# Optimization experiments

Hardware: AMD Instinct MI355X
Metric: run time of the kernel (lower is better)

Reference implementation:

```python
import jax, jax.numpy as jnp
import numpy as np


def setup_inputs() -> dict:
    key = jax.random.key(0)
    k1, k2, k3, k4, k5 = jax.random.split(key, 5)
    N, M, K = 200000, 50, 4
    T = 1000.0
    ti = jnp.sort(jax.random.uniform(k1, (N,), dtype=jnp.float32) * T)
    mi = jax.random.randint(k2, (N,), 0, M, dtype=jnp.int64)
    mu_at_events = jax.random.uniform(k3, (N,), dtype=jnp.float32) * 0.5 + 0.05
    alpha = jax.random.uniform(k4, (K, M, M), dtype=jnp.float32) * 0.1
    gamma = jax.random.uniform(k5, (K,), dtype=jnp.float32) * 2.0 + 0.5
    return {"ti": ti, "mi": mi, "mu_at_events": mu_at_events, "alpha": alpha, "gamma": gamma}


def _hawkes_logsum(ti, mi, mu_at_events, alpha, gamma):
    # ti: [N] sorted event times; mi: [N] event types in [0, M)
    # alpha: [K, M, M]; gamma: [K]; mu_at_events: [N]
    N = ti.shape[0]
    M = alpha.shape[1]
    # inter-event gaps; dt[0] = 0 so the first event has zero excitation state
    dt = jnp.concatenate([jnp.zeros((1,), ti.dtype), ti[1:] - ti[:-1]])  # [N]
    a = jnp.exp(-gamma[None, :] * dt[:, None])  # [N, K] decay factors
    # one-hot of the PREVIOUS event's type (row 0 is all-zero, matching e_mi)
    prev_onehot = jnp.zeros((N, M), ti.dtype).at[jnp.arange(1, N), mi[:-1]].set(1.0)
    b = a[:, None, :] * prev_onehot[:, :, None]  # [N, M, K]

    # linear recurrence S_i = a_i * S_{i-1} + b_i via associative scan
    # combine((a1,b1),(a2,b2)) = (a1*a2, a2*b1 + b2)
    def combine(x, y):
        a1, b1 = x
        a2, b2 = y
        return (a1 * a2, a2[:, None, :] * b1 + b2)

    _, S = jax.lax.associative_scan(combine, (a, b))  # S: [N, M, K]
    # S[i, m, k] = sum_{j < i, m_j = m} exp(-gamma_k (t_i - t_j))
    alpha_at = alpha[:, mi, :]  # [K, N, M] rows of alpha for each event's type
    lam = mu_at_events + jnp.einsum('knm,nmk,k->n', alpha_at, S, gamma)  # [N]
    return jnp.sum(jnp.log(lam))


def reference(ti, mi, mu_at_events, alpha, gamma):
    return _hawkes_logsum(ti, mi, mu_at_events, alpha, gamma)
```

## Files before the change

### kernel.cpp

```cpp
#include <hip/hip_runtime.h>

#define CHUNK 256
#define MM 50
#define KK 4
#define STATE 200
#define ASTRIDE 51
#define SUP 32
#define NSMAX 26
#define GMAX 1024

__device__ int   g_ticket;
__device__ float g_chunkB[GMAX * STATE];
__device__ float g_superB[64 * STATE];

__device__ __forceinline__ unsigned short f2bf(float x) {
  unsigned u = __float_as_uint(x);
  u += 0x7fffu + ((u >> 16) & 1u);
  return (unsigned short)(u >> 16);
}
__device__ __forceinline__ float bflo(unsigned u) { return __uint_as_float(u << 16); }
__device__ __forceinline__ float bfhi(unsigned u) { return __uint_as_float(u & 0xffff0000u); }

__device__ __forceinline__ void st_agent(float* p, float v) {
  __hip_atomic_store(p, v, __ATOMIC_RELAXED, __HIP_MEMORY_SCOPE_AGENT);
}
__device__ __forceinline__ float ld_agent(const float* p) {
  return __hip_atomic_load(p, __ATOMIC_RELAXED, __HIP_MEMORY_SCOPE_AGENT);
}

__global__ __launch_bounds__(512) void hawkes_df(
    const float* __restrict__ ti, const int* __restrict__ mi,
    const float* __restrict__ mu, const float* __restrict__ alpha,
    const float* __restrict__ gamma, float* __restrict__ out,
    int N, int G, int NB) {
  int tid = threadIdx.x;
  __shared__ int vid_s;
  __shared__ unsigned P0[MM * ASTRIDE];
  __shared__ unsigned P1[MM * ASTRIDE];
  __shared__ __align__(16) float4 Fj[512];
  __shared__ int   cj[512];
  __shared__ __align__(16) float Q[16][STATE];
  __shared__ float SB1[STATE];
  __shared__ float SB2[STATE];
  __shared__ float teL[SUP];
  __shared__ float tlast[NSMAX];
  __shared__ float red8[8];

  if (tid == 0) vid_s = atomicAdd(&g_ticket, 1);

  int b = blockIdx.x;
  int c0 = 2 * b;
  int lQ = c0 * CHUNK;
  int sup = b >> 4;
  int g0c = sup * SUP;
  int nloc = c0 - g0c;
  int ch = tid >> 8;

  float gk0 = gamma[0], gk1 = gamma[1], gk2 = gamma[2], gk3 = gamma[3];

  for (int i = tid; i < 16 * STATE; i += 512) ((float*)Q)[i] = 0.f;
  if (tid < SUP) {
    int c = g0c + tid;
    if (c < G) teL[tid] = ti[min(N, (c + 1) * CHUNK) - 1];
  } else if (tid >= 64 && tid < 64 + NSMAX) {
    int s = tid - 64;
    if (s < sup) tlast[s] = ti[min(N, (s + 1) * SUP * CHUNK) - 1];
  }
  if (b == 0 && tid == 0) st_agent(out, 0.f);

  float tref0 = ti[(b == 0) ? 0 : (lQ - 1)];
  float tref_ch = ch ? ti[min(N - 1, lQ + CHUNK - 1)] : tref0;
  int n = lQ + tid;
  bool has_n = (n < N);
  float ti_n = has_n ? ti[n] : 0.f;
  int   mi_n = has_n ? mi[n] : 0;
  float mu_n = has_n ? mu[n] : 0.f;
  int j = lQ - 1 + tid;
  float ti_j = __shfl_up(ti_n, 1, 64);
  int   mi_j = __shfl_up(mi_n, 1, 64);
  if ((tid & 63) == 0 && j >= 0) { ti_j = ti[j]; mi_j = mi[j]; }
  bool valid = (j >= 0) && has_n;
  int myc = valid ? mi_j : 0;
  float4 F = make_float4(0.f, 0.f, 0.f, 0.f);
  if (valid) {
    float tj = ti_j - tref_ch;
    F = make_float4(__expf(gk0 * tj), __expf(gk1 * tj),
                    __expf(gk2 * tj), __expf(gk3 * tj));
  }
  cj[tid] = myc;
  Fj[tid] = F;
  __syncthreads();

  if (valid) {
    float* q = &Q[tid >> 5][myc * KK];
    atomicAdd(q + 0, F.x); atomicAdd(q + 1, F.y);
    atomicAdd(q + 2, F.z); atomicAdd(q + 3, F.w);
  }
  #pragma unroll
  for (int u = 0; u < 5; ++u) {
    int idx = tid + 512 * u;
    if (idx < MM * MM) {
      int c = idx / MM, cp = idx - c * MM;
      float a0 = gk0 * alpha[idx];
      float a1 = gk1 * alpha[2500 + idx];
      float a2 = gk2 * alpha[5000 + idx];
      float a3 = gk3 * alpha[7500 + idx];
      P0[c * ASTRIDE + cp] = (unsigned)f2bf(a0) | ((unsigned)f2bf(a1) << 16);
      P1[c * ASTRIDE + cp] = (unsigned)f2bf(a2) | ((unsigned)f2bf(a3) << 16);
    }
  }
  __syncthreads();

  float epoch_s = ((vid_s / NB) & 1) ? -1.f : 1.f;
  float gkc = (tid & 2) ? ((tid & 1) ? gk3 : gk2) : ((tid & 1) ? gk1 : gk0);
  float totA = 0.f, totB = 0.f, dA = 0.f, dB = 0.f;
  if (tid < STATE) {
    #pragma unroll
    for (int q = 0; q < 8; ++q)  totA += Q[q][tid];
    #pragma unroll
    for (int q = 8; q < 16; ++q) totB += Q[q][tid];
    dA = __expf(-gkc * (teL[nloc] - tref0));
    dB = __expf(-gkc * (teL[nloc + 1] - teL[nloc]));
    st_agent(&g_chunkB[(size_t)c0 * STATE + tid], epoch_s * (dA * totA + 1.f));
    st_agent(&g_chunkB[(size_t)(c0 + 1) * STATE + tid], epoch_s * (dB * totB + 1.f));
  }

  float4 acc = make_float4(0.f, 0.f, 0.f, 0.f);
  if (has_n) {
    int rowb = mi_n * ASTRIDE;
    int base = tid & ~31;
    #pragma unroll 4
    for (int s = base; s <= tid; ++s) {
      unsigned p0 = P0[rowb + cj[s]];
      unsigned p1 = P1[rowb + cj[s]];
      float4 f = Fj[s];
      acc.x += bflo(p0) * f.x; acc.y += bfhi(p0) * f.y;
      acc.z += bflo(p1) * f.z; acc.w += bfhi(p1) * f.w;
    }
  }

  bool closer = ((b & 15) == 15) || (b == NB - 1);
  bool grpA = (tid < STATE);
  bool grpB = (tid >= 256) && (tid < 256 + STATE);
  int st = tid & 255;
  float SA = 0.f;
  int cpar = nloc >> 1;
  int cse = (sup + 1) >> 1, cso = sup >> 1;

  float rc[15], rs[13];
  if (grpA) {
    #pragma unroll
    for (int i = 0; i < 15; ++i)
      rc[i] = (i < cpar) ? ld_agent(&g_chunkB[(size_t)(g0c + 2 * i) * STATE + st]) : epoch_s;
    #pragma unroll
    for (int i = 0; i < 13; ++i)
      rs[i] = (i < cse) ? ld_agent(&g_superB[(size_t)(2 * i) * STATE + st]) : epoch_s;
  } else if (grpB) {
    #pragma unroll
    for (int i = 0; i < 15; ++i)
      rc[i] = (i < cpar) ? ld_agent(&g_chunkB[(size_t)(g0c + 2 * i + 1) * STATE + st]) : epoch_s;
    #pragma unroll
    for (int i = 0; i < 13; ++i)
      rs[i] = (i < cso) ? ld_agent(&g_superB[(size_t)(2 * i + 1) * STATE + st]) : epoch_s;
  }
  if (grpA) {
    #pragma unroll
    for (int i = 0; i < 15; ++i) if (i < cpar) {
      float v = rc[i];
      while (epoch_s * v < 0.5f) {
        __builtin_amdgcn_s_sleep(1);
        v = ld_agent(&g_chunkB[(size_t)(g0c + 2 * i) * STATE + st]);
      }
      SA += __expf(-gkc * (tref0 - teL[2 * i])) * (epoch_s * v - 1.f);
    }
  } else if (grpB) {
    float PB = 0.f;
    #pragma unroll
    for (int i = 0; i < 15; ++i) if (i < cpar) {
      float v = rc[i];
      while (epoch_s * v < 0.5f) {
        __builtin_amdgcn_s_sleep(1);
        v = ld_agent(&g_chunkB[(size_t)(g0c + 2 * i + 1) * STATE + st]);
      }
      PB += __expf(-gkc * (tref0 - teL[2 * i + 1])) * (epoch_s * v - 1.f);
    }
    SB1[st] = PB;
  }

  if (closer) __syncthreads();
  if (closer && grpA) {
    float Sin = SA + SB1[st];
    float run2 = dA * (Sin + totA);
    run2 = dB * (run2 + totB);
    st_agent(&g_superB[(size_t)sup * STATE + st], epoch_s * (run2 + 1.f));
    SA = Sin;
  }

  if (grpA) {
    #pragma unroll
    for (int i = 0; i < 13; ++i) if (i < cse) {
      float v = rs[i];
      while (epoch_s * v < 0.5f) {
        __builtin_amdgcn_s_sleep(1);
        v = ld_agent(&g_superB[(size_t)(2 * i) * STATE + st]);
      }
      SA += __expf(-gkc * (tref0 - tlast[2 * i])) * (epoch_s * v - 1.f);
    }
  } else if (grpB) {
    float PB2 = 0.f;
    #pragma unroll
    for (int i = 0; i < 13; ++i) if (i < cso) {
      float v = rs[i];
      while (epoch_s * v < 0.5f) {
        __builtin_amdgcn_s_sleep(1);
        v = ld_agent(&g_superB[(size_t)(2 * i + 1) * STATE + st]);
      }
      PB2 += __expf(-gkc * (tref0 - tlast[2 * i + 1])) * (epoch_s * v - 1.f);
    }
    SB2[st] = PB2;
  }
  __syncthreads();

  if (grpA) {
    float S = SA + SB2[st] + (closer ? 0.f : SB1[st]);
    float run = S;
    #pragma unroll
    for (int q = 0; q < 8; ++q)  { float t = Q[q][st]; Q[q][st] = run; run += t; }
    run = dA * run;
    #pragma unroll
    for (int q = 8; q < 16; ++q) { float t = Q[q][st]; Q[q][st] = run; run += t; }
  }
  __syncthreads();

  float local = 0.f;
  if (has_n) {
    int rowb = mi_n * ASTRIDE;
    const float4* wb = (const float4*)&Q[tid >> 5][0];
    #pragma unroll 10
    for (int m = 0; m < MM; ++m) {
      unsigned p0 = P0[rowb + m];
      unsigned p1 = P1[rowb + m];
      float4 w = wb[m];
      acc.x += bflo(p0) * w.x; acc.y += bfhi(p0) * w.y;
      acc.z += bflo(p1) * w.z; acc.w += bfhi(p1) * w.w;
    }
    float tn = ti_n - tref_ch;
    float lam = mu_n
              + __expf(-gk0 * tn) * acc.x + __expf(-gk1 * tn) * acc.y
              + __expf(-gk2 * tn) * acc.z + __expf(-gk3 * tn) * acc.w;
    local = __logf(lam);
  }
  #pragma unroll
  for (int off = 32; off > 0; off >>= 1)
    local += __shfl_down(local, off, 64);
  if ((tid & 63) == 0) red8[tid >> 6] = local;
  __syncthreads();
  if (tid == 0) {
    float acc8 = 0.f;
    #pragma unroll
    for (int w = 0; w < 8; ++w) acc8 += red8[w];
    atomicAdd(out, acc8);
  }
}

extern "C" void kernel_launch(void* const* d_in, const int* in_sizes, int n_in,
                              void* d_out, int out_size, void* d_ws, size_t ws_size,
                              hipStream_t stream) {
  const float* ti    = (const float*)d_in[0];
  const int*   mi    = (const int*)d_in[1];
  const float* mu    = (const float*)d_in[2];
  const float* alpha = (const float*)d_in[3];
  const float* gamma = (const float*)d_in[4];
  float* out = (float*)d_out;
  int N = in_sizes[0];
  int G = (N + CHUNK - 1) / CHUNK;
  if (G > GMAX) return;
  int NB = (G + 1) / 2;

  hawkes_df<<<NB, 512, 0, stream>>>(ti, mi, mu, alpha, gamma, out, N, G, NB);
}
```

Before: 85.70 us.

## Decouple local chunk work from cross-block carry wait via linearity split

Computes the in-chunk exclusive prefix of Q with zero carry-in and runs the 50-term per-event alpha contraction before waiting on predecessor blocks, except for closer blocks, which must wait first. The incoming carry state is applied afterwards through a separate per-(type,k) contraction of alpha with the carry, held in new shared arrays RA and RB, and each event adds that term. This moves the bulk of each block's compute off the critical path of the decoupled look-back chain. In exchange it adds an extra 200-thread 50-step contraction, more shared memory and extra barriers.

```diff
diff --git a/kernel.cpp b/kernel.cpp
--- a/kernel.cpp
+++ b/kernel.cpp
@@ -42,6 +42,8 @@
   __shared__ __align__(16) float Q[16][STATE];
   __shared__ float SB1[STATE];
   __shared__ float SB2[STATE];
+  __shared__ __align__(16) float RA[MM * 20];
+  __shared__ __align__(16) float RB[MM * 20];
   __shared__ float teL[SUP];
   __shared__ float tlast[NSMAX];
   __shared__ float red8[8];
@@ -113,21 +115,54 @@
 
   float epoch_s = ((vid_s / NB) & 1) ? -1.f : 1.f;
   float gkc = (tid & 2) ? ((tid & 1) ? gk3 : gk2) : ((tid & 1) ? gk1 : gk0);
+  bool closer = ((b & 15) == 15) || (b == NB - 1);
+  bool grpA = (tid < STATE);
+  bool grpB = (tid >= 256) && (tid < 256 + STATE);
+  int st = tid & 255;
+  int cpar = nloc >> 1;
+  int cse = (sup + 1) >> 1, cso = sup >> 1;
+
   float totA = 0.f, totB = 0.f, dA = 0.f, dB = 0.f;
-  if (tid < STATE) {
-    #pragma unroll
-    for (int q = 0; q < 8; ++q)  totA += Q[q][tid];
-    #pragma unroll
-    for (int q = 8; q < 16; ++q) totB += Q[q][tid];
+  if (grpA) {
+    #pragma unroll
+    for (int q = 0; q < 8; ++q)  totA += Q[q][st];
+    #pragma unroll
+    for (int q = 8; q < 16; ++q) totB += Q[q][st];
     dA = __expf(-gkc * (teL[nloc] - tref0));
     dB = __expf(-gkc * (teL[nloc + 1] - teL[nloc]));
-    st_agent(&g_chunkB[(size_t)c0 * STATE + tid], epoch_s * (dA * totA + 1.f));
-    st_agent(&g_chunkB[(size_t)(c0 + 1) * STATE + tid], epoch_s * (dB * totB + 1.f));
+    st_agent(&g_chunkB[(size_t)c0 * STATE + st], epoch_s * (dA * totA + 1.f));
+    st_agent(&g_chunkB[(size_t)(c0 + 1) * STATE + st], epoch_s * (dB * totB + 1.f));
+  }
+
+  float rc[15], rs[13];
+  if (grpA) {
+    #pragma unroll
+    for (int i = 0; i < 15; ++i)
+      rc[i] = (i < cpar) ? ld_agent(&g_chunkB[(size_t)(g0c + 2 * i) * STATE + st]) : epoch_s;
+    #pragma unroll
+    for (int i = 0; i < 13; ++i)
+      rs[i] = (i < cse) ? ld_agent(&g_superB[(size_t)(2 * i) * STATE + st]) : epoch_s;
+  } else if (grpB) {
+    #pragma unroll
+    for (int i = 0; i < 15; ++i)
+      rc[i] = (i < cpar) ? ld_agent(&g_chunkB[(size_t)(g0c + 2 * i + 1) * STATE + st]) : epoch_s;
+    #pragma unroll
+    for (int i = 0; i < 13; ++i)
+      rs[i] = (i < cso) ? ld_agent(&g_superB[(size_t)(2 * i + 1) * STATE + st]) : epoch_s;
+  }
+
+  if (grpA) {
+    float run = 0.f;
+    #pragma unroll
+    for (int q = 0; q < 8; ++q)  { float t = Q[q][st]; Q[q][st] = run; run += t; }
+    run = dA * run;
+    #pragma unroll
+    for (int q = 8; q < 16; ++q) { float t = Q[q][st]; Q[q][st] = run; run += t; }
   }
 
   float4 acc = make_float4(0.f, 0.f, 0.f, 0.f);
+  int rowb = mi_n * ASTRIDE;
   if (has_n) {
-    int rowb = mi_n * ASTRIDE;
     int base = tid & ~31;
     #pragma unroll 4
     for (int s = base; s <= tid; ++s) {
@@ -139,102 +174,43 @@
     }
   }
 
-  bool closer = ((b & 15) == 15) || (b == NB - 1);
-  bool grpA = (tid < STATE);
-  bool grpB = (tid >= 256) && (tid < 256 + STATE);
-  int st = tid & 255;
   float SA = 0.f;
-  int cpar = nloc >> 1;
-  int cse = (sup + 1) >> 1, cso = sup >> 1;
-
-  float rc[15], rs[13];
-  if (grpA) {
-    #pragma unroll
-    for (int i = 0; i < 15; ++i)
-      rc[i] = (i < cpar) ? ld_agent(&g_chunkB[(size_t)(g0c + 2 * i) * STATE + st]) : epoch_s;
-    #pragma unroll
-    for (int i = 0; i < 13; ++i)
-      rs[i] = (i < cse) ? ld_agent(&g_superB[(size_t)(2 * i) * STATE + st]) : epoch_s;
-  } else if (grpB) {
-    #pragma unroll
-    for (int i = 0; i < 15; ++i)
-      rc[i] = (i < cpar) ? ld_agent(&g_chunkB[(size_t)(g0c + 2 * i + 1) * STATE + st]) : epoch_s;
-    #pragma unroll
-    for (int i = 0; i < 13; ++i)
-      rs[i] = (i < cso) ? ld_agent(&g_superB[(size_t)(2 * i + 1) * STATE + st]) : epoch_s;
-  }
-  if (grpA) {
-    #pragma unroll
-    for (int i = 0; i < 15; ++i) if (i < cpar) {
-      float v = rc[i];
-      while (epoch_s * v < 0.5f) {
-        __builtin_amdgcn_s_sleep(1);
-        v = ld_agent(&g_chunkB[(size_t)(g0c + 2 * i) * STATE + st]);
-      }
-      SA += __expf(-gkc * (tref0 - teL[2 * i])) * (epoch_s * v - 1.f);
-    }
-  } else if (grpB) {
-    float PB = 0.f;
-    #pragma unroll
-    for (int i = 0; i < 15; ++i) if (i < cpar) {
-      float v = rc[i];
-      while (epoch_s * v < 0.5f) {
-        __builtin_amdgcn_s_sleep(1);
-        v = ld_agent(&g_chunkB[(size_t)(g0c + 2 * i + 1) * STATE + st]);
-      }
-      PB += __expf(-gkc * (tref0 - teL[2 * i + 1])) * (epoch_s * v - 1.f);
-    }
-    SB1[st] = PB;
-  }
-
-  if (closer) __syncthreads();
-  if (closer && grpA) {
-    float Sin = SA + SB1[st];
-    float run2 = dA * (Sin + totA);
-    run2 = dB * (run2 + totB);
-    st_agent(&g_superB[(size_t)sup * STATE + st], epoch_s * (run2 + 1.f));
-    SA = Sin;
-  }
-
-  if (grpA) {
-    #pragma unroll
-    for (int i = 0; i < 13; ++i) if (i < cse) {
-      float v = rs[i];
-      while (epoch_s * v < 0.5f) {
-        __builtin_amdgcn_s_sleep(1);
-        v = ld_agent(&g_superB[(size_t)(2 * i) * STATE + st]);
-      }
-      SA += __expf(-gkc * (tref0 - tlast[2 * i])) * (epoch_s * v - 1.f);
-    }
-  } else if (grpB) {
-    float PB2 = 0.f;
-    #pragma unroll
-    for (int i = 0; i < 13; ++i) if (i < cso) {
-      float v = rs[i];
-      while (epoch_s * v < 0.5f) {
-        __builtin_amdgcn_s_sleep(1);
-        v = ld_agent(&g_superB[(size_t)(2 * i + 1) * STATE + st]);
-      }
-      PB2 += __expf(-gkc * (tref0 - tlast[2 * i + 1])) * (epoch_s * v - 1.f);
-    }
-    SB2[st] = PB2;
-  }
-  __syncthreads();
-
-  if (grpA) {
-    float S = SA + SB2[st] + (closer ? 0.f : SB1[st]);
-    float run = S;
-    #pragma unroll
-    for (int q = 0; q < 8; ++q)  { float t = Q[q][st]; Q[q][st] = run; run += t; }
-    run = dA * run;
-    #pragma unroll
-    for (int q = 8; q < 16; ++q) { float t = Q[q][st]; Q[q][st] = run; run += t; }
-  }
-  __syncthreads();
-
-  float local = 0.f;
+  if (closer) {
+    if (grpA) {
+      #pragma unroll
+      for (int i = 0; i < 15; ++i) if (i < cpar) {
+        float v = rc[i];
+        while (epoch_s * v < 0.5f) {
+          __builtin_amdgcn_s_sleep(1);
+          v = ld_agent(&g_chunkB[(size_t)(g0c + 2 * i) * STATE + st]);
+        }
+        SA += __expf(-gkc * (tref0 - teL[2 * i])) * (epoch_s * v - 1.f);
+      }
+    } else if (grpB) {
+      float PB = 0.f;
+      #pragma unroll
+      for (int i = 0; i < 15; ++i) if (i < cpar) {
+        float v = rc[i];
+        while (epoch_s * v < 0.5f) {
+          __builtin_amdgcn_s_sleep(1);
+          v = ld_agent(&g_chunkB[(size_t)(g0c + 2 * i + 1) * STATE + st]);
+        }
+        PB += __expf(-gkc * (tref0 - teL[2 * i + 1])) * (epoch_s * v - 1.f);
+      }
+      SB1[st] = PB;
+    }
+    __syncthreads();
+    if (grpA) {
+      float Sin = SA + SB1[st];
+      float run2 = dA * (Sin + totA);
+      run2 = dB * (run2 + totB);
+      st_agent(&g_superB[(size_t)sup * STATE + st], epoch_s * (run2 + 1.f));
+      SA = Sin;
+    }
+  }
+  __syncthreads();
+
   if (has_n) {
-    int rowb = mi_n * ASTRIDE;
     const float4* wb = (const float4*)&Q[tid >> 5][0];
     #pragma unroll 10
     for (int m = 0; m < MM; ++m) {
@@ -244,10 +220,98 @@
       acc.x += bflo(p0) * w.x; acc.y += bfhi(p0) * w.y;
       acc.z += bflo(p1) * w.z; acc.w += bfhi(p1) * w.w;
     }
+  }
+
+  if (!closer) {
+    if (grpA) {
+      #pragma unroll
+      for (int i = 0; i < 15; ++i) if (i < cpar) {
+        float v = rc[i];
+        while (epoch_s * v < 0.5f) {
+          __builtin_amdgcn_s_sleep(1);
+          v = ld_agent(&g_chunkB[(size_t)(g0c + 2 * i) * STATE + st]);
+        }
+        SA += __expf(-gkc * (tref0 - teL[2 * i])) * (epoch_s * v - 1.f);
+      }
+    } else if (grpB) {
+      float PB = 0.f;
+      #pragma unroll
+      for (int i = 0; i < 15; ++i) if (i < cpar) {
+        float v = rc[i];
+        while (epoch_s * v < 0.5f) {
+          __builtin_amdgcn_s_sleep(1);
+          v = ld_agent(&g_chunkB[(size_t)(g0c + 2 * i + 1) * STATE + st]);
+        }
+        PB += __expf(-gkc * (tref0 - teL[2 * i + 1])) * (epoch_s * v - 1.f);
+      }
+      SB1[st] = PB;
+    }
+  }
+  if (grpA) {
+    #pragma unroll
+    for (int i = 0; i < 13; ++i) if (i < cse) {
+      float v = rs[i];
+      while (epoch_s * v < 0.5f) {
+        __builtin_amdgcn_s_sleep(1);
+        v = ld_agent(&g_superB[(size_t)(2 * i) * STATE + st]);
+      }
+      SA += __expf(-gkc * (tref0 - tlast[2 * i])) * (epoch_s * v - 1.f);
+    }
+  } else if (grpB) {
+    float PB2 = 0.f;
+    #pragma unroll
+    for (int i = 0; i < 13; ++i) if (i < cso) {
+      float v = rs[i];
+      while (epoch_s * v < 0.5f) {
+        __builtin_amdgcn_s_sleep(1);
+        v = ld_agent(&g_superB[(size_t)(2 * i + 1) * STATE + st]);
+      }
+      PB2 += __expf(-gkc * (tref0 - tlast[2 * i + 1])) * (epoch_s * v - 1.f);
+    }
+    SB2[st] = PB2;
+  }
+  __syncthreads();
+
+  if (grpA) {
+    float S = SA + SB2[st] + (closer ? 0.f : SB1[st]);
+    SB1[st] = S;
+    SB2[st] = dA * S;
+  }
+  __syncthreads();
+
+  if (tid < STATE) {
+    int c = tid >> 2, k = tid & 3;
+    float rv = 0.f;
+    #pragma unroll 10
+    for (int m = 0; m < MM; ++m) {
+      unsigned w = (k & 2) ? P1[c * ASTRIDE + m] : P0[c * ASTRIDE + m];
+      float pv = (k & 1) ? bfhi(w) : bflo(w);
+      rv += pv * SB1[m * KK + k];
+    }
+    RA[c * 20 + k] = rv;
+  } else if (tid >= 256 && tid < 256 + STATE) {
+    int c = st >> 2, k = st & 3;
+    float rv = 0.f;
+    #pragma unroll 10
+    for (int m = 0; m < MM; ++m) {
+      unsigned w = (k & 2) ? P1[c * ASTRIDE + m] : P0[c * ASTRIDE + m];
+      float pv = (k & 1) ? bfhi(w) : bflo(w);
+      rv += pv * SB2[m * KK + k];
+    }
+    RB[c * 20 + k] = rv;
+  }
+  __syncthreads();
+
+  float local = 0.f;
+  if (has_n) {
+    const float* Rx = (tid < 256) ? RA : RB;
+    float4 rv = *(const float4*)&Rx[mi_n * 20];
     float tn = ti_n - tref_ch;
     float lam = mu_n
-              + __expf(-gk0 * tn) * acc.x + __expf(-gk1 * tn) * acc.y
-              + __expf(-gk2 * tn) * acc.z + __expf(-gk3 * tn) * acc.w;
+              + __expf(-gk0 * tn) * (acc.x + rv.x)
+              + __expf(-gk1 * tn) * (acc.y + rv.y)
+              + __expf(-gk2 * tn) * (acc.z + rv.z)
+              + __expf(-gk3 * tn) * (acc.w + rv.w);
     local = __logf(lam);
   }
   #pragma unroll
```

Result: slower. 89.55 us (+4.5%).
